# Kernel tuning notes

Hardware: AMD Instinct MI355X
Metric: run time of the kernel (lower is better)

## Reference

```python
import jax, jax.numpy as jnp
import numpy as np

N = 100000
E = 1600000
IN_DIM = 128
HID = 64
HEADS = 4
OUT_DIM = 64
NEG_SLOPE = 0.2


def _xavier(key, shape):
    fan_in, fan_out = shape[0], shape[1]
    limit = float(np.sqrt(6.0 / (fan_in + fan_out)))
    return jax.random.uniform(key, shape, jnp.float32, -limit, limit)


def setup_inputs() -> dict:
    key = jax.random.key(0)
    ks = jax.random.split(key, 8)
    x = jax.random.normal(ks[0], (N, IN_DIM), jnp.float32)
    edge_index = jax.random.randint(ks[1], (2, E), 0, N, dtype=jnp.int32)
    # Layer 0: in=128 -> heads=4, out=64, concat
    W0 = _xavier(ks[2], (IN_DIM, HEADS * HID))
    a0 = _xavier(ks[3], (HEADS, 2 * HID))
    # Layer 1: in=256 -> heads=4, out=64, concat
    W1 = _xavier(ks[4], (HEADS * HID, HEADS * HID))
    a1 = _xavier(ks[5], (HEADS, 2 * HID))
    # Layer 2 (output): in=256 -> heads=1, out=64, no concat
    W2 = _xavier(ks[6], (HEADS * HID, 1 * OUT_DIM))
    a2 = _xavier(ks[7], (1, 2 * OUT_DIM))
    return {"x": x, "edge_index": edge_index,
            "W0": W0, "a0": a0, "W1": W1, "a1": a1, "W2": W2, "a2": a2}


def gat_layer(x, src, dst, W, a, heads, out_dim, concat):
    n = x.shape[0]
    h = (x @ W).reshape(n, heads, out_dim)            # [N, H, D]
    a_s, a_d = a[:, :out_dim], a[:, out_dim:]          # [H, D] each
    alpha_s = jnp.einsum('nhd,hd->nh', h, a_s)         # [N, H]
    alpha_d = jnp.einsum('nhd,hd->nh', h, a_d)         # [N, H]
    e = jax.nn.leaky_relu(alpha_s[src] + alpha_d[dst], NEG_SLOPE)  # [E, H]
    # segment softmax over edges grouped by destination node
    e_max = jax.lax.stop_gradient(jax.ops.segment_max(e, dst, num_segments=n))
    e_max = jnp.where(jnp.isfinite(e_max), e_max, 0.0)
    e_exp = jnp.exp(e - e_max[dst])                    # [E, H]
    denom = jax.ops.segment_sum(e_exp, dst, num_segments=n)  # [N, H]
    att = e_exp / (denom[dst] + 1e-16)                 # [E, H]
    msg = h[src] * att[:, :, None]                     # [E, H, D]
    out = jax.ops.segment_sum(msg, dst, num_segments=n)  # [N, H, D]
    if concat:
        return out.reshape(n, heads * out_dim)
    return out.mean(axis=1)


def reference(x, edge_index, W0, a0, W1, a1, W2, a2):
    src, dst = edge_index[0], edge_index[1]
    # layer 0 + ELU (dropout is identity in eval mode)
    h = gat_layer(x, src, dst, W0, a0, HEADS, HID, True)
    h = jax.nn.elu(h)
    # layer 1 + ELU
    h = gat_layer(h, src, dst, W1, a1, HEADS, HID, True)
    h = jax.nn.elu(h)
    # output layer: single head, no concat, no activation
    out = gat_layer(h, src, dst, W2, a2, 1, OUT_DIM, False)
    return out
```

## Files before the change

### kernel.cpp

```cpp
#include <hip/hip_runtime.h>
#include <math.h>

#define NEG_SLOPE 0.2f

typedef short short8 __attribute__((ext_vector_type(8)));
typedef float float4v __attribute__((ext_vector_type(4)));
typedef _Float16 h8 __attribute__((ext_vector_type(8)));

__device__ __forceinline__ unsigned short f2bf(float f) {
    unsigned u = __float_as_uint(f);
    unsigned r = (u + 0x7fff + ((u >> 16) & 1)) >> 16;
    return (unsigned short)r;
}
__device__ __forceinline__ float bf2f(unsigned short h) {
    return __uint_as_float(((unsigned)h) << 16);
}
__device__ __forceinline__ unsigned short f2h(float f) {
    _Float16 t = (_Float16)f;
    return *(unsigned short*)&t;
}

__device__ __forceinline__ void gload_lds16(const void* g, void* l) {
    __builtin_amdgcn_global_load_lds(
        (const __attribute__((address_space(1))) unsigned int*)g,
        (__attribute__((address_space(3))) unsigned int*)l, 16, 0, 0);
}


__global__ void count_kernel(const int* __restrict__ dst, int E, int* __restrict__ counts) {
    int i = blockIdx.x * blockDim.x + threadIdx.x;
    if (i < E) atomicAdd(&counts[dst[i]], 1);
}

__global__ void scan1_kernel(const int* __restrict__ in, int n, int* __restrict__ bsums) {
    __shared__ int sdata[256];
    int tid = threadIdx.x;
    int base = blockIdx.x * 1024 + tid * 4;
    int s = 0;
#pragma unroll
    for (int j = 0; j < 4; ++j) if (base + j < n) s += in[base + j];
    sdata[tid] = s; __syncthreads();
    for (int off = 128; off > 0; off >>= 1) {
        if (tid < off) sdata[tid] += sdata[tid + off];
        __syncthreads();
    }
    if (tid == 0) bsums[blockIdx.x] = sdata[0];
}

__global__ void scan2_kernel(int* bsums, int nb) {
    __shared__ int sd[128];
    int tid = threadIdx.x;
    int v = (tid < nb) ? bsums[tid] : 0;
    sd[tid] = v; __syncthreads();
    for (int off = 1; off < 128; off <<= 1) {
        int t = (tid >= off) ? sd[tid - off] : 0;
        __syncthreads();
        sd[tid] += t;
        __syncthreads();
    }
    if (tid < nb) bsums[tid] = sd[tid] - v;
}

__global__ void scan3_kernel(const int* __restrict__ in, int n, const int* __restrict__ bsums,
                             int* __restrict__ row_ptr, int* __restrict__ cursor, int E) {
    __shared__ int sdata[256];
    int tid = threadIdx.x;
    int base = blockIdx.x * 1024 + tid * 4;
    int v[4]; int s = 0;
#pragma unroll
    for (int j = 0; j < 4; ++j) { v[j] = (base + j < n) ? in[base + j] : 0; s += v[j]; }
    sdata[tid] = s; __syncthreads();
    for (int off = 1; off < 256; off <<= 1) {
        int t = (tid >= off) ? sdata[tid - off] : 0;
        __syncthreads();
        sdata[tid] += t;
        __syncthreads();
    }
    int excl = sdata[tid] - s;
    int run = bsums[blockIdx.x] + excl;
#pragma unroll
    for (int j = 0; j < 4; ++j) {
        if (base + j < n) { row_ptr[base + j] = run; cursor[base + j] = run; run += v[j]; }
    }
    if (blockIdx.x == 0 && tid == 0) row_ptr[n] = E;
}

__global__ void fill_kernel(const int* __restrict__ dst, const int* __restrict__ src, int E,
                            int* __restrict__ cursor, int* __restrict__ sperm) {
    int i = blockIdx.x * blockDim.x + threadIdx.x;
    if (i < E) {
        int p = atomicAdd(&cursor[dst[i]], 1);
        sperm[p] = src[i];
    }
}


__global__ __launch_bounds__(256) void prep_kernel(
    const float* __restrict__ W0, const float* __restrict__ W1, const float* __restrict__ W2,
    const float* __restrict__ a0, const float* __restrict__ a1, const float* __restrict__ a2,
    unsigned short* __restrict__ WT0, unsigned short* __restrict__ WT1, unsigned short* __restrict__ WT2,
    unsigned short* __restrict__ wa0, unsigned short* __restrict__ wa1, unsigned short* __restrict__ wa2) {
    int i = blockIdx.x * 256 + threadIdx.x;
    if (i < 32768) {
        int k = i >> 8, n = i & 255;
        WT0[n * 128 + k] = f2bf(W0[i]);
    } else if (i < 98304) {
        int j = i - 32768;
        int k = j >> 8, n = j & 255;
        WT1[n * 256 + k] = f2bf(W1[j]);
    } else if (i < 114688) {
        int j = i - 98304;
        int k = j >> 6, n = j & 63;
        WT2[n * 256 + k] = f2bf(W2[j]);
    } else if (i < 114688 + 2048) {
        int t = i - 114688;
        int k = t >> 4, j8 = t & 15;
        float s = 0.f;
        if (j8 < 8) {
            int h = j8 & 3, off = (j8 >> 2) * 64;
            for (int d = 0; d < 64; ++d)
                s += W0[k * 256 + h * 64 + d] * a0[h * 128 + off + d];
        }
        wa0[j8 * 128 + k] = f2bf(s);
    } else if (i < 114688 + 2048 + 4096) {
        int t = i - 114688 - 2048;
        int k = t >> 4, j8 = t & 15;
        float s = 0.f;
        if (j8 < 8) {
            int h = j8 & 3, off = (j8 >> 2) * 64;
            for (int d = 0; d < 64; ++d)
                s += W1[k * 256 + h * 64 + d] * a1[h * 128 + off + d];
        }
        wa1[j8 * 256 + k] = f2bf(s);
    } else if (i < 114688 + 2048 + 4096 + 4096) {
        int t = i - 114688 - 2048 - 4096;
        int k = t >> 4, j8 = t & 15;
        float s = 0.f;
        if (j8 < 2) {
            for (int d = 0; d < 64; ++d)
                s += W2[k * 64 + d] * a2[j8 * 64 + d];
        }
        wa2[j8 * 256 + k] = f2bf(s);
    }
}

__global__ void xcvt_kernel(const float* __restrict__ X, unsigned short* __restrict__ b, int total) {
    int i = blockIdx.x * 256 + threadIdx.x;
    if (i >= total) return;
    b[i] = f2bf(X[i]);
}


template <int BN>
__global__ __launch_bounds__(256) void gemm_fused(
    const unsigned short* __restrict__ A, const unsigned short* __restrict__ WT,
    const unsigned short* __restrict__ waSDT,
    unsigned short* __restrict__ hf16,
    float* __restrict__ as_, float* __restrict__ ad_,
    int M, int K) {
    __shared__ unsigned short AL[128 * 32];
    __shared__ unsigned short BL[BN * 32];
    __shared__ unsigned short WaL[16 * 32];

    int t = threadIdx.x;
    int w = t >> 6, lane = t & 63;
    int q = lane >> 4, i16 = lane & 15;
    int rowBase = blockIdx.x * 128;
    int colBase = blockIdx.y * BN;

    constexpr int MT = (BN == 128) ? 4 : 2;
    int wrow = (BN == 128) ? (w >> 1) * 64 : w * 32;
    int wcol = (BN == 128) ? (w & 1) * 64 : 0;

    bool alphaBlk = (blockIdx.y == 0);
    bool alphaWave = alphaBlk && ((BN == 64) || ((w & 1) == 0));

    float4v acc[MT][4];
    float4v accA[MT];
#pragma unroll
    for (int mt = 0; mt < MT; ++mt) {
        accA[mt] = (float4v)(0.f);
#pragma unroll
        for (int nt = 0; nt < 4; ++nt) acc[mt][nt] = (float4v)(0.f);
    }

    int srow = t >> 2;
    int skq = (t & 3) * 8;

    for (int k0 = 0; k0 < K; k0 += 32) {
        gload_lds16(A + (size_t)(rowBase + srow) * K + k0 + skq, AL + w * 512);
        gload_lds16(A + (size_t)(rowBase + 64 + srow) * K + k0 + skq, AL + 2048 + w * 512);
        gload_lds16(WT + (size_t)(colBase + srow) * K + k0 + skq, BL + w * 512);
        if (BN == 128)
            gload_lds16(WT + (size_t)(colBase + 64 + srow) * K + k0 + skq, BL + 2048 + w * 512);
        if (alphaBlk && w == 0)
            gload_lds16(waSDT + (size_t)srow * K + k0 + skq, WaL);
        __syncthreads();

        short8 af[MT], bf[4];
#pragma unroll
        for (int mt = 0; mt < MT; ++mt)
            af[mt] = *(short8*)&AL[(wrow + mt * 16 + i16) * 32 + q * 8];
#pragma unroll
        for (int nt = 0; nt < 4; ++nt)
            bf[nt] = *(short8*)&BL[(wcol + nt * 16 + i16) * 32 + q * 8];
#pragma unroll
        for (int mt = 0; mt < MT; ++mt)
#pragma unroll
            for (int nt = 0; nt < 4; ++nt)
                acc[mt][nt] = __builtin_amdgcn_mfma_f32_16x16x32_bf16(af[mt], bf[nt], acc[mt][nt], 0, 0, 0);
        if (alphaWave) {
            short8 aw = *(short8*)&WaL[i16 * 32 + q * 8];
#pragma unroll
            for (int mt = 0; mt < MT; ++mt)
                accA[mt] = __builtin_amdgcn_mfma_f32_16x16x32_bf16(af[mt], aw, accA[mt], 0, 0, 0);
        }
        __syncthreads();
    }

    int cb0 = colBase + wcol;
#pragma unroll
    for (int mt = 0; mt < MT; ++mt)
#pragma unroll
        for (int r = 0; r < 4; ++r) {
            int grow = rowBase + wrow + mt * 16 + q * 4 + r;
            bool ok = grow < M;
            if (ok) {
#pragma unroll
                for (int nt = 0; nt < 4; ++nt) {
                    float v = acc[mt][nt][r];
                    if (BN == 128) hf16[(size_t)grow * 256 + cb0 + nt * 16 + i16] = f2h(v);
                    else           hf16[(size_t)grow * 64 + nt * 16 + i16] = f2h(v);
                }
                if (alphaWave) {
                    float av = accA[mt][r];
                    if (BN == 128) {
                        if (i16 < 4)      as_[grow * 4 + i16] = av;
                        else if (i16 < 8) ad_[grow * 4 + (i16 - 4)] = av;
                    } else {
                        if (i16 == 0)      as_[grow] = av;
                        else if (i16 == 1) ad_[grow] = av;
                    }
                }
            }
        }
}


__global__ __launch_bounds__(256) void aggregate4(
    const unsigned short* __restrict__ hf16, const int* __restrict__ row_ptr,
    const int* __restrict__ sperm, const float* __restrict__ as_, const float* __restrict__ ad_,
    unsigned short* __restrict__ outB, int n) {
    int w = threadIdx.x >> 6, lane = threadIdx.x & 63;
    int node = blockIdx.x * 4 + w;
    if (node >= n) return;
    int beg = row_ptr[node], end = row_ptr[node + 1];
    int deg = end - beg;
    int myh = lane & 3;
    float ad_my = ad_[node * 4 + myh];

    int half = lane >> 5;
    int dg = lane & 31;
    int hh = dg >> 3;
    float acc[8];
#pragma unroll
    for (int k = 0; k < 8; ++k) acc[k] = 0.f;
    float lsum = 0.f;

    const char* hbase = (const char*)hf16;
    unsigned dgo = (unsigned)dg << 4;

    for (int el0 = 0; el0 < deg; el0 += 16) {
        int ne = deg - el0; if (ne > 16) ne = 16;
        int eSlot = lane >> 2;
        float att = 0.f; int sMy = 0;
        if (eSlot < ne) {
            sMy = __builtin_nontemporal_load(&sperm[beg + el0 + eSlot]);
            float e = as_[sMy * 4 + myh] + ad_my;
            e = e > 0.f ? e : NEG_SLOPE * e;
            att = __expf(e);
        }
        lsum += att;

        int j = 0;
        for (; j + 8 <= ne; j += 8) {
            int sl0 = j + half, sl1 = j + 2 + half, sl2 = j + 4 + half, sl3 = j + 6 + half;
            float a0 = __shfl(att, sl0 * 4 + hh, 64);
            int   s0 = __shfl(sMy, sl0 * 4, 64);
            float a1 = __shfl(att, sl1 * 4 + hh, 64);
            int   s1 = __shfl(sMy, sl1 * 4, 64);
            float a2 = __shfl(att, sl2 * 4 + hh, 64);
            int   s2 = __shfl(sMy, sl2 * 4, 64);
            float a3 = __shfl(att, sl3 * 4 + hh, 64);
            int   s3 = __shfl(sMy, sl3 * 4, 64);
            h8 v0 = *(const h8*)(hbase + (((unsigned)s0 << 9) + dgo));
            h8 v1 = *(const h8*)(hbase + (((unsigned)s1 << 9) + dgo));
            h8 v2 = *(const h8*)(hbase + (((unsigned)s2 << 9) + dgo));
            h8 v3 = *(const h8*)(hbase + (((unsigned)s3 << 9) + dgo));
#pragma unroll
            for (int k = 0; k < 8; ++k) acc[k] += a0 * (float)v0[k];
#pragma unroll
            for (int k = 0; k < 8; ++k) acc[k] += a1 * (float)v1[k];
#pragma unroll
            for (int k = 0; k < 8; ++k) acc[k] += a2 * (float)v2[k];
#pragma unroll
            for (int k = 0; k < 8; ++k) acc[k] += a3 * (float)v3[k];
        }
        for (; j < ne; j += 2) {
            int sl = j + half;
            float a = __shfl(att, sl * 4 + hh, 64);
            int   s = __shfl(sMy, sl * 4, 64);
            h8 v = *(const h8*)(hbase + (((unsigned)s << 9) + dgo));
#pragma unroll
            for (int k = 0; k < 8; ++k) acc[k] += a * (float)v[k];
        }
    }

#pragma unroll
    for (int m = 4; m < 64; m <<= 1) lsum += __shfl_xor(lsum, m, 64);
    float inv = 1.f / (lsum + 1e-16f);
    float invh = __shfl(inv, hh, 64);

#pragma unroll
    for (int k = 0; k < 8; ++k) {
        acc[k] += __shfl_xor(acc[k], 32, 64);
        acc[k] *= invh;
    }

    if (half == 0) {
        short8 hv;
#pragma unroll
        for (int k = 0; k < 8; ++k) {
            float o = acc[k] > 0.f ? acc[k] : (__expf(acc[k]) - 1.f);
            hv[k] = (short)f2bf(o);
        }
        __builtin_nontemporal_store(hv, (short8*)(outB + (size_t)node * 256 + dg * 8));
    }
}


__global__ __launch_bounds__(256) void aggregate1(
    const unsigned short* __restrict__ hf16, const int* __restrict__ row_ptr,
    const int* __restrict__ sperm, const float* __restrict__ as_, const float* __restrict__ ad_,
    float* __restrict__ out, int n) {
    int w = threadIdx.x >> 6, lane = threadIdx.x & 63;
    int node = blockIdx.x * 4 + w;
    if (node >= n) return;
    int beg = row_ptr[node], end = row_ptr[node + 1];
    int deg = end - beg;
    float ad_n = ad_[node];

    int eg = lane >> 3;
    int dg = lane & 7;
    float acc[8];
#pragma unroll
    for (int k = 0; k < 8; ++k) acc[k] = 0.f;
    float lsum = 0.f;

    const char* hbase = (const char*)hf16;
    unsigned dgo = (unsigned)dg << 4;

    for (int el0 = 0; el0 < deg; el0 += 64) {
        int ne = deg - el0; if (ne > 64) ne = 64;
        float att = 0.f; int sMy = 0;
        if (lane < ne) {
            sMy = __builtin_nontemporal_load(&sperm[beg + el0 + lane]);
            float e = as_[sMy] + ad_n;
            e = e > 0.f ? e : NEG_SLOPE * e;
            att = __expf(e);
        }
        lsum += att;

        int j = 0;
        for (; j + 32 <= ne; j += 32) {
            int sl0 = j + eg, sl1 = j + 8 + eg, sl2 = j + 16 + eg, sl3 = j + 24 + eg;
            float a0 = __shfl(att, sl0, 64);
            int   s0 = __shfl(sMy, sl0, 64);
            float a1 = __shfl(att, sl1, 64);
            int   s1 = __shfl(sMy, sl1, 64);
            float a2 = __shfl(att, sl2, 64);
            int   s2 = __shfl(sMy, sl2, 64);
            float a3 = __shfl(att, sl3, 64);
            int   s3 = __shfl(sMy, sl3, 64);
            h8 v0 = *(const h8*)(hbase + (((unsigned)s0 << 7) + dgo));
            h8 v1 = *(const h8*)(hbase + (((unsigned)s1 << 7) + dgo));
            h8 v2 = *(const h8*)(hbase + (((unsigned)s2 << 7) + dgo));
            h8 v3 = *(const h8*)(hbase + (((unsigned)s3 << 7) + dgo));
#pragma unroll
            for (int k = 0; k < 8; ++k) acc[k] += a0 * (float)v0[k];
#pragma unroll
            for (int k = 0; k < 8; ++k) acc[k] += a1 * (float)v1[k];
#pragma unroll
            for (int k = 0; k < 8; ++k) acc[k] += a2 * (float)v2[k];
#pragma unroll
            for (int k = 0; k < 8; ++k) acc[k] += a3 * (float)v3[k];
        }
        for (; j < ne; j += 8) {
            int sl = j + eg;
            float a = __shfl(att, sl, 64);
            int   s = __shfl(sMy, sl, 64);
            h8 v = *(const h8*)(hbase + (((unsigned)s << 7) + dgo));
#pragma unroll
            for (int k = 0; k < 8; ++k) acc[k] += a * (float)v[k];
        }
    }

#pragma unroll
    for (int m = 1; m < 64; m <<= 1) lsum += __shfl_xor(lsum, m, 64);
    float inv = 1.f / (lsum + 1e-16f);

#pragma unroll
    for (int m = 8; m < 64; m <<= 1)
#pragma unroll
        for (int k = 0; k < 8; ++k) acc[k] += __shfl_xor(acc[k], m, 64);

    if (eg == 0) {
        float4v o0, o1;
        o0[0] = acc[0] * inv; o0[1] = acc[1] * inv; o0[2] = acc[2] * inv; o0[3] = acc[3] * inv;
        o1[0] = acc[4] * inv; o1[1] = acc[5] * inv; o1[2] = acc[6] * inv; o1[3] = acc[7] * inv;
        __builtin_nontemporal_store(o0, (float4v*)(out + (size_t)node * 64 + dg * 8));
        __builtin_nontemporal_store(o1, (float4v*)(out + (size_t)node * 64 + dg * 8 + 4));
    }
}


extern "C" void kernel_launch(void* const* d_in, const int* in_sizes, int n_in,
                              void* d_out, int out_size, void* d_ws, size_t ws_size,
                              hipStream_t stream) {
    const float* x  = (const float*)d_in[0];
    const int*   ei = (const int*)d_in[1];
    const float* W0 = (const float*)d_in[2];
    const float* a0 = (const float*)d_in[3];
    const float* W1 = (const float*)d_in[4];
    const float* a1 = (const float*)d_in[5];
    const float* W2 = (const float*)d_in[6];
    const float* a2 = (const float*)d_in[7];
    float* out = (float*)d_out;

    int N = in_sizes[0] / 128;
    int E = in_sizes[1] / 2;
    int Npad = (N + 127) & ~127;
    const int* srcp = ei;
    const int* dstp = ei + E;

    char* ws = (char*)d_ws;
    size_t off = 0;
    auto alloc = [&](size_t bytes) -> void* {
        void* p = ws + off;
        off += (bytes + 255) & ~(size_t)255;
        return p;
    };
    unsigned short* xbf  = (unsigned short*)alloc((size_t)Npad * 128 * 2);
    unsigned short* actB = (unsigned short*)alloc((size_t)Npad * 256 * 2);
    unsigned short* hf16 = (unsigned short*)alloc((size_t)Npad * 256 * 2);
    unsigned short* Cf16 = (unsigned short*)alloc((size_t)Npad * 64 * 2);
    float* as_    = (float*)alloc((size_t)N * 4 * 4);
    float* ad_    = (float*)alloc((size_t)N * 4 * 4);
    int*   counts = (int*)alloc((size_t)N * 4);
    int*   row_ptr= (int*)alloc((size_t)(N + 1) * 4);
    int*   cursor = (int*)alloc((size_t)N * 4);
    int*   sperm  = (int*)alloc((size_t)E * 4);
    unsigned short* WT0 = (unsigned short*)alloc((size_t)256 * 128 * 2);
    unsigned short* WT1 = (unsigned short*)alloc((size_t)256 * 256 * 2);
    unsigned short* WT2 = (unsigned short*)alloc((size_t)64 * 256 * 2);
    unsigned short* wa0 = (unsigned short*)alloc((size_t)16 * 128 * 2);
    unsigned short* wa1 = (unsigned short*)alloc((size_t)16 * 256 * 2);
    unsigned short* wa2 = (unsigned short*)alloc((size_t)16 * 256 * 2);
    int*   bsums  = (int*)alloc(4096);

    hipMemsetAsync(counts, 0, (size_t)N * 4, stream);
    int egrid = (E + 255) / 256;
    count_kernel<<<egrid, 256, 0, stream>>>(dstp, E, counts);
    int nb = (N + 1023) / 1024;
    scan1_kernel<<<nb, 256, 0, stream>>>(counts, N, bsums);
    scan2_kernel<<<1, 128, 0, stream>>>(bsums, nb);
    scan3_kernel<<<nb, 256, 0, stream>>>(counts, N, bsums, row_ptr, cursor, E);
    fill_kernel<<<egrid, 256, 0, stream>>>(dstp, srcp, E, cursor, sperm);

    prep_kernel<<<(114688 + 10240 + 255) / 256, 256, 0, stream>>>(
        W0, W1, W2, a0, a1, a2, WT0, WT1, WT2, wa0, wa1, wa2);
    xcvt_kernel<<<((N * 128) + 255) / 256, 256, 0, stream>>>(x, xbf, N * 128);

    int gemm_gx = Npad / 128;
    int ngrid4 = (N + 3) / 4;

    gemm_fused<128><<<dim3(gemm_gx, 2), 256, 0, stream>>>(xbf, WT0, wa0, hf16, as_, ad_, N, 128);
    aggregate4<<<ngrid4, 256, 0, stream>>>(hf16, row_ptr, sperm, as_, ad_, actB, N);

    gemm_fused<128><<<dim3(gemm_gx, 2), 256, 0, stream>>>(actB, WT1, wa1, hf16, as_, ad_, N, 256);
    aggregate4<<<ngrid4, 256, 0, stream>>>(hf16, row_ptr, sperm, as_, ad_, actB, N);

    gemm_fused<64><<<dim3(gemm_gx, 1), 256, 0, stream>>>(actB, WT2, wa2, Cf16, as_, ad_, N, 256);
    aggregate1<<<ngrid4, 256, 0, stream>>>(Cf16, row_ptr, sperm, as_, ad_, out, N);
}
```

Baseline: 705.9 us.

## Replace global-atomic CSR build with two-level bucketed counting sort

Builds the destination-sorted CSR with chunked LDS histograms over 512-node buckets, a global scan, and a scatter of (dst,src) pairs into buckets. A per-bucket kernel then does the fine counting sort in shared memory. This removes the random global atomics of the old count and fill kernels. In exchange it writes an extra 8-byte-per-edge temporary buffer and adds launches.

Result: faster. 574.9 us, median of 2 (-18.6%).

```diff
diff --git a/kernel.cpp b/kernel.cpp
--- a/kernel.cpp
+++ b/kernel.cpp
@@ -2,9 +2,11 @@
 #include <math.h>
 
 #define NEG_SLOPE 0.2f
+#define SCHUNK 4096
 
 typedef short short8 __attribute__((ext_vector_type(8)));
 typedef float float4v __attribute__((ext_vector_type(4)));
+typedef int int2v __attribute__((ext_vector_type(2)));
 typedef _Float16 h8 __attribute__((ext_vector_type(8)));
 
 __device__ __forceinline__ unsigned short f2bf(float f) {
@@ -27,9 +29,19 @@
 }
 
 
-__global__ void count_kernel(const int* __restrict__ dst, int E, int* __restrict__ counts) {
-    int i = blockIdx.x * blockDim.x + threadIdx.x;
-    if (i < E) atomicAdd(&counts[dst[i]], 1);
+__global__ __launch_bounds__(256) void hist_kernel(const int* __restrict__ dst, int E,
+                                                   int NBUCK, int B1, int* __restrict__ H) {
+    __shared__ int hist[256];
+    int tid = threadIdx.x;
+    for (int j = tid; j < NBUCK; j += 256) hist[j] = 0;
+    __syncthreads();
+    int base = blockIdx.x * SCHUNK;
+    int endi = base + SCHUNK; if (endi > E) endi = E;
+    for (int i = base + tid; i < endi; i += 256)
+        atomicAdd(&hist[dst[i] >> 9], 1);
+    __syncthreads();
+    for (int j = tid; j < NBUCK; j += 256)
+        H[j * B1 + blockIdx.x] = hist[j];
 }
 
 __global__ void scan1_kernel(const int* __restrict__ in, int n, int* __restrict__ bsums) {
@@ -61,8 +73,8 @@
     if (tid < nb) bsums[tid] = sd[tid] - v;
 }
 
-__global__ void scan3_kernel(const int* __restrict__ in, int n, const int* __restrict__ bsums,
-                             int* __restrict__ row_ptr, int* __restrict__ cursor, int E) {
+__global__ void scan3g_kernel(const int* __restrict__ in, int n, const int* __restrict__ bsums,
+                              int* __restrict__ outs) {
     __shared__ int sdata[256];
     int tid = threadIdx.x;
     int base = blockIdx.x * 1024 + tid * 4;
@@ -80,17 +92,66 @@
     int run = bsums[blockIdx.x] + excl;
 #pragma unroll
     for (int j = 0; j < 4; ++j) {
-        if (base + j < n) { row_ptr[base + j] = run; cursor[base + j] = run; run += v[j]; }
-    }
-    if (blockIdx.x == 0 && tid == 0) row_ptr[n] = E;
-}
-
-__global__ void fill_kernel(const int* __restrict__ dst, const int* __restrict__ src, int E,
-                            int* __restrict__ cursor, int* __restrict__ sperm) {
-    int i = blockIdx.x * blockDim.x + threadIdx.x;
-    if (i < E) {
-        int p = atomicAdd(&cursor[dst[i]], 1);
-        sperm[p] = src[i];
+        if (base + j < n) { outs[base + j] = run; run += v[j]; }
+    }
+}
+
+__global__ __launch_bounds__(256) void scatter_kernel(
+    const int* __restrict__ dst, const int* __restrict__ src, int E,
+    int NBUCK, int B1, const int* __restrict__ Hs, int2v* __restrict__ tmp) {
+    __shared__ int curs[256];
+    int tid = threadIdx.x;
+    for (int j = tid; j < NBUCK; j += 256) curs[j] = Hs[j * B1 + blockIdx.x];
+    __syncthreads();
+    int base = blockIdx.x * SCHUNK;
+    int endi = base + SCHUNK; if (endi > E) endi = E;
+    for (int i = base + tid; i < endi; i += 256) {
+        int d = dst[i], sv = src[i];
+        int p = atomicAdd(&curs[d >> 9], 1);
+        int2v pr; pr[0] = d; pr[1] = sv;
+        tmp[p] = pr;
+    }
+}
+
+__global__ __launch_bounds__(256) void bucket_kernel(
+    const int2v* __restrict__ tmp, const int* __restrict__ Hs,
+    int B1, int NBUCK, int E, int n,
+    int* __restrict__ row_ptr, int* __restrict__ sperm) {
+    int b = blockIdx.x, tid = threadIdx.x;
+    int s = Hs[b * B1];
+    int e = (b + 1 < NBUCK) ? Hs[(b + 1) * B1] : E;
+    int base = b << 9;
+    __shared__ int hist[512];
+    __shared__ int scanv[512];
+    __shared__ int psum[256];
+    hist[tid] = 0; hist[tid + 256] = 0;
+    __syncthreads();
+    for (int i = s + tid; i < e; i += 256)
+        atomicAdd(&hist[tmp[i][0] - base], 1);
+    __syncthreads();
+    int a = hist[2 * tid], c = hist[2 * tid + 1];
+    psum[tid] = a + c;
+    __syncthreads();
+    for (int off = 1; off < 256; off <<= 1) {
+        int t = (tid >= off) ? psum[tid - off] : 0;
+        __syncthreads();
+        psum[tid] += t;
+        __syncthreads();
+    }
+    int excl = psum[tid] - (a + c);
+    scanv[2 * tid] = excl;
+    scanv[2 * tid + 1] = excl + a;
+    __syncthreads();
+    for (int j = tid; j < 512; j += 256) {
+        int node = base + j;
+        if (node < n) row_ptr[node] = s + scanv[j];
+    }
+    if (b == 0 && tid == 0) row_ptr[n] = E;
+    __syncthreads();
+    for (int i = s + tid; i < e; i += 256) {
+        int2v pr = tmp[i];
+        int p = s + atomicAdd(&scanv[pr[0] - base], 1);
+        sperm[p] = pr[1];
     }
 }
 
@@ -456,9 +517,7 @@
     unsigned short* Cf16 = (unsigned short*)alloc((size_t)Npad * 64 * 2);
     float* as_    = (float*)alloc((size_t)N * 4 * 4);
     float* ad_    = (float*)alloc((size_t)N * 4 * 4);
-    int*   counts = (int*)alloc((size_t)N * 4);
     int*   row_ptr= (int*)alloc((size_t)(N + 1) * 4);
-    int*   cursor = (int*)alloc((size_t)N * 4);
     int*   sperm  = (int*)alloc((size_t)E * 4);
     unsigned short* WT0 = (unsigned short*)alloc((size_t)256 * 128 * 2);
     unsigned short* WT1 = (unsigned short*)alloc((size_t)256 * 256 * 2);
@@ -468,14 +527,20 @@
     unsigned short* wa2 = (unsigned short*)alloc((size_t)16 * 256 * 2);
     int*   bsums  = (int*)alloc(4096);
 
-    hipMemsetAsync(counts, 0, (size_t)N * 4, stream);
-    int egrid = (E + 255) / 256;
-    count_kernel<<<egrid, 256, 0, stream>>>(dstp, E, counts);
-    int nb = (N + 1023) / 1024;
-    scan1_kernel<<<nb, 256, 0, stream>>>(counts, N, bsums);
-    scan2_kernel<<<1, 128, 0, stream>>>(bsums, nb);
-    scan3_kernel<<<nb, 256, 0, stream>>>(counts, N, bsums, row_ptr, cursor, E);
-    fill_kernel<<<egrid, 256, 0, stream>>>(dstp, srcp, E, cursor, sperm);
+    int B1 = (E + SCHUNK - 1) / SCHUNK;
+    int NBUCK = (N + 511) >> 9;
+    int Hn = NBUCK * B1;
+    int*   H   = (int*)alloc((size_t)Hn * 4);
+    int*   Hs  = (int*)alloc((size_t)Hn * 4);
+    int2v* tmp = (int2v*)alloc((size_t)E * 8);
+
+    hist_kernel<<<B1, 256, 0, stream>>>(dstp, E, NBUCK, B1, H);
+    int nbH = (Hn + 1023) / 1024;
+    scan1_kernel<<<nbH, 256, 0, stream>>>(H, Hn, bsums);
+    scan2_kernel<<<1, 128, 0, stream>>>(bsums, nbH);
+    scan3g_kernel<<<nbH, 256, 0, stream>>>(H, Hn, bsums, Hs);
+    scatter_kernel<<<B1, 256, 0, stream>>>(dstp, srcp, E, NBUCK, B1, Hs, tmp);
+    bucket_kernel<<<NBUCK, 256, 0, stream>>>(tmp, Hs, B1, NBUCK, E, N, row_ptr, sperm);
 
     prep_kernel<<<(114688 + 10240 + 255) / 256, 256, 0, stream>>>(
         W0, W1, W2, a0, a1, a2, WT0, WT1, WT2, wa0, wa1, wa2);
```
